# Kernel tuning notes

Measured on AMD Instinct MI355X. Metric: run time of the kernel, lower is better.

## Reference

```python
import jax, jax.numpy as jnp
import numpy as np

IN_CH, OUT_CH, HEADS, DIM = 256, 256, 8, 64

def _xavier(key, shape, fan_in, fan_out):
    upper = np.sqrt(6.0) / np.sqrt(float(fan_in + fan_out))
    return jax.random.uniform(key, shape, jnp.float32) * (2.0 * upper) - upper

def setup_inputs() -> dict:
    key = jax.random.key(0)
    kf, kq, kk, kv, ko = jax.random.split(key, 5)
    features = jax.random.normal(kf, (8, 1024, IN_CH), jnp.float32)
    weight_q = _xavier(kq, (IN_CH, HEADS, DIM), IN_CH, HEADS * DIM)
    weight_k = _xavier(kk, (IN_CH, HEADS, DIM), IN_CH, HEADS * DIM)
    weight_v = _xavier(kv, (IN_CH, HEADS, DIM), IN_CH, HEADS * DIM)
    weight_out = _xavier(ko, (OUT_CH, HEADS, DIM), HEADS * DIM, OUT_CH)
    return {"features": features, "weight_q": weight_q, "weight_k": weight_k,
            "weight_v": weight_v, "weight_out": weight_out}

def reference(features, weight_q, weight_k, weight_v, weight_out):
    # QKV projections: (b,n,c) x (c,h,d) -> (b,n,h,d)
    q = jnp.einsum('bnc,chd->bnhd', features, weight_q)
    k = jnp.einsum('bnc,chd->bnhd', features, weight_k)
    v = jnp.einsum('bnc,chd->bnhd', features, weight_v)
    # Scores: (b, i=query, j=key, h)
    qk = jnp.einsum('bihd,bjhd->bijh', q, k) / jnp.sqrt(jnp.asarray(DIM, q.dtype))
    # NOTE: original softmaxes over dim=1, i.e. the QUERY axis (faithful quirk)
    qk_softmax = jax.nn.softmax(qk, axis=1)
    # Original broadcasts v over j, so combination = v[b,i,h,d] * sum_j softmax[b,i,j,h]
    attn_weight = jnp.sum(qk_softmax, axis=2)  # (b, i, h)
    applied = v * attn_weight[:, :, :, None]   # (b, i, h, d)
    out = jnp.einsum('bihd,ohd->bio', applied, weight_out)
    return out
```

## Files before the change

### kernel.cpp

```cpp
#include <hip/hip_runtime.h>
#include <hip/hip_bf16.h>
#include <cstdint>


typedef __attribute__((ext_vector_type(8))) short bf16x8;
typedef __attribute__((ext_vector_type(4))) float f32x4;

#define EXP2(x) __builtin_amdgcn_exp2f(x)
#define MFMA(a, b, c) __builtin_amdgcn_mfma_f32_16x16x32_bf16((a), (b), (c), 0, 0, 0)
#define QSCALE 0.18033688011112042f

static __device__ __forceinline__ uint32_t pk2(float x, float y) {
  union { __hip_bfloat162 h; uint32_t u; } c;
  c.h = __float22bfloat162_rn(float2{x, y});
  return c.u;
}
static __device__ __forceinline__ short cvt1(float f) {
  union { __hip_bfloat16 h; short s; } c;
  c.h = __float2bfloat16(f);
  return c.s;
}

__global__ __launch_bounds__(256) void k_prep(
    const float* __restrict__ F,  const float* __restrict__ Wq,
    const float* __restrict__ Wk, const float* __restrict__ Wv,
    const float* __restrict__ Wo,
    short* __restrict__ Fb, short* __restrict__ Wtf, short* __restrict__ Wobf)
{
  const int gt = blockIdx.x * 256 + threadIdx.x;
  if (gt < 262144) {
    const int b  = gt >> 15;
    const int r  = gt & 32767;
    const int c8 = r & 31;
    const int i  = r >> 5;
    const float* src = F + ((size_t)(b * 1024 + i)) * 256 + c8 * 8;
    const float4 v0 = *(const float4*)src;
    const float4 v1 = *(const float4*)(src + 4);
    uint32_t u[4] = {pk2(v0.x, v0.y), pk2(v0.z, v0.w),
                     pk2(v1.x, v1.y), pk2(v1.z, v1.w)};
    const int strip = i >> 4, lo = i & 15;
    const int s = c8 >> 3, kk = (c8 >> 2) & 1, hi = c8 & 3;
    *(uint4*)&Fb[(size_t)b * 262144 + (size_t)strip * 4096 + s * 1024 +
                 kk * 512 + (hi * 16 + lo) * 8] = *(uint4*)u;
  } else if (gt < 311296) {
    const int wt = gt - 262144;
    const int m  = wt >> 14;
    const int r  = wt & 16383;
    const int n  = r & 511;
    const int c8 = r >> 9;
    const float* W = (m == 0) ? Wq : (m == 1) ? Wk : Wv;
    const float scale = (m == 0) ? QSCALE : 1.0f;
    short tmp[8];
#pragma unroll
    for (int j = 0; j < 8; ++j)
      tmp[j] = cvt1(W[(size_t)(c8 * 8 + j) * 512 + n] * scale);
    const int h = n >> 6, fm = (n >> 4) & 3, lo = n & 15;
    const int s = c8 >> 3, kk = (c8 >> 2) & 1, hi = c8 & 3;
    *(int4*)&Wtf[(size_t)(((m * 8 + h) * 4 + fm) * 4 + s) * 1024 +
                 kk * 512 + (hi * 16 + lo) * 8] = *(int4*)tmp;
  } else if (gt < 327680) {
    const int wo = gt - 311296;
    const int o  = wo >> 6;
    const int k8 = wo & 63;
    const float* src = Wo + (size_t)o * 512 + k8 * 8;
    const float4 v0 = *(const float4*)src;
    const float4 v1 = *(const float4*)(src + 4);
    uint32_t u[4] = {pk2(v0.x, v0.y), pk2(v0.z, v0.w),
                     pk2(v1.x, v1.y), pk2(v1.z, v1.w)};
    const int nt = o >> 6, fc = (o >> 4) & 3, lo = o & 15;
    const int s = k8 >> 3, kk = (k8 >> 2) & 1, hi = k8 & 3;
    *(uint4*)&Wobf[(size_t)((nt * 4 + fc) * 8 + s) * 1024 +
                   kk * 512 + (hi * 16 + lo) * 8] = *(uint4*)u;
  }
}

__global__ __launch_bounds__(256, 4) void k_qkv(
    const short* __restrict__ Fb, const short* __restrict__ Wtf,
    short* __restrict__ Qf, short* __restrict__ Kf, short* __restrict__ Vf)
{
  const int hw = blockIdx.x, t = threadIdx.x;
  const int xcd  = hw & 7;
  const int slot = hw >> 3;
  const int mh   = slot >> 3;
  const int g    = xcd * 8 + (slot & 7);
  const int m    = mh >> 3;
  const int h    = mh & 7;
  const int b    = g >> 3;
  const int mt   = g & 7;
  const int wv = t >> 6, l = t & 63, lo = l & 15, hi = l >> 4;

  f32x4 acc[4][2];
#pragma unroll
  for (int i = 0; i < 4; ++i)
#pragma unroll
    for (int j = 0; j < 2; ++j) acc[i][j] = (f32x4){0.f, 0.f, 0.f, 0.f};

  const short* fbase = Fb + (size_t)b * 262144;
  const short* wbase = Wtf + (size_t)(m * 8 + h) * 16384;
  const int strip0 = mt * 8 + wv * 2;

#pragma unroll
  for (int s = 0; s < 4; ++s) {
    bf16x8 bb[2][2];
#pragma unroll
    for (int fn = 0; fn < 2; ++fn)
#pragma unroll
      for (int kk = 0; kk < 2; ++kk)
        bb[fn][kk] = *(const bf16x8*)(fbase + (size_t)(strip0 + fn) * 4096 +
                                      s * 1024 + kk * 512 + l * 8);
#pragma unroll
    for (int fm = 0; fm < 4; ++fm) {
      const short* wr = wbase + (size_t)(fm * 4 + s) * 1024 + l * 8;
      bf16x8 a0 = *(const bf16x8*)(wr);
      bf16x8 a1 = *(const bf16x8*)(wr + 512);
      acc[fm][0] = MFMA(a0, bb[0][0], acc[fm][0]);
      acc[fm][1] = MFMA(a0, bb[1][0], acc[fm][1]);
      acc[fm][0] = MFMA(a1, bb[0][1], acc[fm][0]);
      acc[fm][1] = MFMA(a1, bb[1][1], acc[fm][1]);
    }
  }

  short* O = (m == 0) ? Qf : (m == 1) ? Kf : Vf;
  const size_t obase = (size_t)(b * 8 + h) * 65536;
#pragma unroll
  for (int fm = 0; fm < 4; ++fm)
#pragma unroll
    for (int fn = 0; fn < 2; ++fn) {
      uint32_t u[2] = {pk2(acc[fm][fn][0], acc[fm][fn][1]),
                       pk2(acc[fm][fn][2], acc[fm][fn][3])};
      const int strip = strip0 + fn;
      const int kk = fm >> 1;
      const int hip = (fm & 1) * 2 + (hi >> 1);
      const int e0 = (hi & 1) * 4;
      *(uint2*)&O[obase + (size_t)strip * 1024 + kk * 512 +
                  (hip * 16 + lo) * 8 + e0] = *(uint2*)u;
    }
}

template <int NSLICE>
__global__ __launch_bounds__(256, 4) void k_attw(
    const short* __restrict__ Qf, const short* __restrict__ Kf,
    float* __restrict__ Wgp)
{
  constexpr int JW = 1024 / NSLICE;
  constexpr int NS = JW / 16;
  __shared__ float Red[4 * JW];
  const int hw = blockIdx.x, t = threadIdx.x;
  const int xcd  = hw & 7;
  const int slot = hw >> 3;
  const int bh   = xcd * 8 + slot / NSLICE;
  const int jb   = slot % NSLICE;
  const size_t base = (size_t)bh * 65536;
  const int wv = t >> 6, l = t & 63, lo = l & 15, hi = l >> 4;
  const short* qb = Qf + base;
  const short* kb = Kf + base;

  bf16x8 bk[NS][2];
#pragma unroll
  for (int js = 0; js < NS; ++js) {
    const short* kr = kb + (size_t)(jb * NS + js) * 1024 + l * 8;
    bk[js][0] = *(const bf16x8*)(kr);
    bk[js][1] = *(const bf16x8*)(kr + 512);
  }

  float cs[NS];
#pragma unroll
  for (int js = 0; js < NS; ++js) cs[js] = 0.f;

  {
    bf16x8 a0[2], a1[2];
#pragma unroll
    for (int p = 0; p < 2; ++p) {
      const short* q = qb + (size_t)(wv + 4 * p) * 1024 + l * 8;
      a0[p] = *(const bf16x8*)(q);
      a1[p] = *(const bf16x8*)(q + 512);
    }
#pragma unroll 1
    for (int k = 0; k < 8; ++k) {
      bf16x8 n0[2], n1[2];
      if (k < 7) {
#pragma unroll
        for (int p = 0; p < 2; ++p) {
          const short* q = qb + (size_t)(wv + 8 * (k + 1) + 4 * p) * 1024 + l * 8;
          n0[p] = *(const bf16x8*)(q);
          n1[p] = *(const bf16x8*)(q + 512);
        }
      }
#pragma unroll
      for (int js = 0; js < NS; ++js) {
#pragma unroll
        for (int p = 0; p < 2; ++p) {
          f32x4 acc = (f32x4){0.f, 0.f, 0.f, 0.f};
          acc = MFMA(a0[p], bk[js][0], acc);
          acc = MFMA(a1[p], bk[js][1], acc);
#pragma unroll
          for (int r = 0; r < 4; ++r) cs[js] += EXP2(acc[r]);
        }
      }
      if (k < 7) {
#pragma unroll
        for (int p = 0; p < 2; ++p) { a0[p] = n0[p]; a1[p] = n1[p]; }
      }
    }
  }

#pragma unroll
  for (int js = 0; js < NS; ++js) {
    cs[js] += __shfl_xor(cs[js], 16, 64);
    cs[js] += __shfl_xor(cs[js], 32, 64);
  }
  if (hi == 0) {
#pragma unroll
    for (int js = 0; js < NS; ++js) Red[wv * JW + js * 16 + lo] = cs[js];
  }
  __syncthreads();
  if (t < JW) {
    float d = Red[t] + Red[JW + t] + Red[2 * JW + t] + Red[3 * JW + t];
    Red[t] = __builtin_amdgcn_rcpf(d);
  }
  __syncthreads();
  float rjv[NS][4];
#pragma unroll
  for (int js = 0; js < NS; ++js)
#pragma unroll
    for (int r = 0; r < 4; ++r)
      rjv[js][r] = Red[js * 16 + hi * 4 + r];

  {
    bf16x8 a0[2], a1[2];
#pragma unroll
    for (int p = 0; p < 2; ++p) {
      const short* q = qb + (size_t)(wv + 4 * p) * 1024 + l * 8;
      a0[p] = *(const bf16x8*)(q);
      a1[p] = *(const bf16x8*)(q + 512);
    }
#pragma unroll 1
    for (int k = 0; k < 8; ++k) {
      bf16x8 n0[2], n1[2];
      if (k < 7) {
#pragma unroll
        for (int p = 0; p < 2; ++p) {
          const short* q = qb + (size_t)(wv + 8 * (k + 1) + 4 * p) * 1024 + l * 8;
          n0[p] = *(const bf16x8*)(q);
          n1[p] = *(const bf16x8*)(q + 512);
        }
      }
      float w2[2] = {0.f, 0.f};
#pragma unroll
      for (int js = 0; js < NS; ++js) {
#pragma unroll
        for (int p = 0; p < 2; ++p) {
          f32x4 acc = (f32x4){0.f, 0.f, 0.f, 0.f};
          acc = MFMA(bk[js][0], a0[p], acc);
          acc = MFMA(bk[js][1], a1[p], acc);
#pragma unroll
          for (int r = 0; r < 4; ++r)
            w2[p] = fmaf(EXP2(acc[r]), rjv[js][r], w2[p]);
        }
      }
#pragma unroll
      for (int p = 0; p < 2; ++p) {
        w2[p] += __shfl_xor(w2[p], 16, 64);
        w2[p] += __shfl_xor(w2[p], 32, 64);
      }
      if (l < 16) {
#pragma unroll
        for (int p = 0; p < 2; ++p)
          Wgp[(size_t)jb * 65536 + (size_t)bh * 1024 +
              (wv + 8 * k + 4 * p) * 16 + l] = w2[p];
      }
      if (k < 7) {
#pragma unroll
        for (int p = 0; p < 2; ++p) { a0[p] = n0[p]; a1[p] = n1[p]; }
      }
    }
  }
}

template <int NSLICE>
__global__ __launch_bounds__(256, 2) void k_out(
    const short* __restrict__ Vf, const float* __restrict__ Wgp,
    const short* __restrict__ Wobf, float* __restrict__ Out)
{
  __shared__ float Wl[8][64];
  const int hw = blockIdx.x, t = threadIdx.x;
  const int slot = hw >> 3;
  const int g    = (hw & 7) * 16 + (slot >> 2);
  const int nt   = slot & 3;
  const int b    = g >> 4;
  const int mt   = g & 15;
  const int n0   = nt * 64;
  const int m0   = mt * 64;
  const int wv = t >> 6, l = t & 63, lo = l & 15, hi = l >> 4;

#pragma unroll
  for (int e = t; e < 512; e += 256) {
    int s = e >> 6, i2 = e & 63;
    float sum = 0.f;
#pragma unroll
    for (int p = 0; p < NSLICE; ++p)
      sum += Wgp[(size_t)p * 65536 + (size_t)(b * 8 + s) * 1024 + m0 + i2];
    Wl[s][i2] = sum;
  }
  __syncthreads();

  f32x4 acc[4];
#pragma unroll
  for (int j = 0; j < 4; ++j) acc[j] = (f32x4){0.f, 0.f, 0.f, 0.f};

  const int strip = mt * 4 + wv;

#pragma unroll 1
  for (int s = 0; s < 8; ++s) {
    const float w = Wl[s][wv * 16 + lo];
    const short* vt = Vf + (size_t)(b * 8 + s) * 65536 + (size_t)strip * 1024;
#pragma unroll
    for (int kk = 0; kk < 2; ++kk) {
      int4 raw = *(const int4*)(vt + kk * 512 + l * 8);
      uint32_t* u = (uint32_t*)&raw;
      uint32_t o[4];
#pragma unroll
      for (int j = 0; j < 4; ++j) {
        float f0 = __uint_as_float(u[j] << 16) * w;
        float f1 = __uint_as_float(u[j] & 0xffff0000u) * w;
        o[j] = pk2(f0, f1);
      }
      bf16x8 a = *(bf16x8*)o;
#pragma unroll
      for (int fc = 0; fc < 4; ++fc) {
        bf16x8 bfr = *(const bf16x8*)(Wobf + (size_t)((nt * 4 + fc) * 8 + s) * 1024 +
                                      kk * 512 + l * 8);
        acc[fc] = MFMA(a, bfr, acc[fc]);
      }
    }
  }

#pragma unroll
  for (int fc = 0; fc < 4; ++fc)
#pragma unroll
    for (int r = 0; r < 4; ++r) {
      int i = m0 + wv * 16 + hi * 4 + r;
      int o = n0 + fc * 16 + lo;
      Out[(size_t)(b * 1024 + i) * 256 + o] = acc[fc][r];
    }
}

extern "C" void kernel_launch(void* const* d_in, const int* in_sizes, int n_in,
                              void* d_out, int out_size, void* d_ws, size_t ws_size,
                              hipStream_t stream) {
  const float* F  = (const float*)d_in[0];
  const float* Wq = (const float*)d_in[1];
  const float* Wk = (const float*)d_in[2];
  const float* Wv = (const float*)d_in[3];
  const float* Wo = (const float*)d_in[4];
  float* out = (float*)d_out;

  char* ws = (char*)d_ws;
  short* Qf   = (short*)(ws);
  short* Kf   = (short*)(ws + (size_t)(8  << 20));
  short* Vf   = (short*)(ws + (size_t)(16 << 20));
  short* Fb   = (short*)(ws + (size_t)(24 << 20));
  float* Wgp  = (float*)(ws + (size_t)(28 << 20));
  short* Wtf  = (short*)(ws + (size_t)(32 << 20));
  short* Wobf = (short*)(ws + (size_t)(32 << 20) + (768 << 10));

  k_prep<<<dim3(1280), 256, 0, stream>>>(F, Wq, Wk, Wv, Wo, Fb, Wtf, Wobf);
  k_qkv <<<dim3(1536), 256, 0, stream>>>(Fb, Wtf, Qf, Kf, Vf);
  k_attw<16><<<dim3(1024), 256, 0, stream>>>(Qf, Kf, Wgp);
  k_out<16> <<<dim3(512),  256, 0, stream>>>(Vf, Wgp, Wobf, out);
}
```

Baseline: 58.07 us.

## Cache exp scores in LDS instead of recomputing QK in second pass

Result: no change. 57.22 us (median of 3 runs) (-1.5%).

```diff
diff --git a/kernel.cpp b/kernel.cpp
--- a/kernel.cpp
+++ b/kernel.cpp
@@ -138,12 +138,13 @@
 }
 
 template <int NSLICE>
-__global__ __launch_bounds__(256, 4) void k_attw(
+__global__ __launch_bounds__(256, 2) void k_attw(
     const short* __restrict__ Qf, const short* __restrict__ Kf,
     float* __restrict__ Wgp)
 {
   constexpr int JW = 1024 / NSLICE;
   constexpr int NS = JW / 16;
+  __shared__ short E[JW][1032];
   __shared__ float Red[4 * JW];
   const int hw = blockIdx.x, t = threadIdx.x;
   const int xcd  = hw & 7;
@@ -193,8 +194,12 @@
           f32x4 acc = (f32x4){0.f, 0.f, 0.f, 0.f};
           acc = MFMA(a0[p], bk[js][0], acc);
           acc = MFMA(a1[p], bk[js][1], acc);
-#pragma unroll
-          for (int r = 0; r < 4; ++r) cs[js] += EXP2(acc[r]);
+          float e0 = EXP2(acc[0]), e1 = EXP2(acc[1]);
+          float e2 = EXP2(acc[2]), e3 = EXP2(acc[3]);
+          cs[js] += (e0 + e1) + (e2 + e3);
+          uint32_t u[2] = {pk2(e0, e1), pk2(e2, e3)};
+          const int strip = wv + 8 * k + 4 * p;
+          *(uint2*)&E[js * 16 + lo][strip * 16 + hi * 4] = *(uint2*)u;
         }
       }
       if (k < 7) {
@@ -219,61 +224,21 @@
     Red[t] = __builtin_amdgcn_rcpf(d);
   }
   __syncthreads();
-  float rjv[NS][4];
-#pragma unroll
-  for (int js = 0; js < NS; ++js)
-#pragma unroll
-    for (int r = 0; r < 4; ++r)
-      rjv[js][r] = Red[js * 16 + hi * 4 + r];
 
   {
-    bf16x8 a0[2], a1[2];
-#pragma unroll
-    for (int p = 0; p < 2; ++p) {
-      const short* q = qb + (size_t)(wv + 4 * p) * 1024 + l * 8;
-      a0[p] = *(const bf16x8*)(q);
-      a1[p] = *(const bf16x8*)(q + 512);
-    }
-#pragma unroll 1
-    for (int k = 0; k < 8; ++k) {
-      bf16x8 n0[2], n1[2];
-      if (k < 7) {
-#pragma unroll
-        for (int p = 0; p < 2; ++p) {
-          const short* q = qb + (size_t)(wv + 8 * (k + 1) + 4 * p) * 1024 + l * 8;
-          n0[p] = *(const bf16x8*)(q);
-          n1[p] = *(const bf16x8*)(q + 512);
-        }
-      }
-      float w2[2] = {0.f, 0.f};
-#pragma unroll
-      for (int js = 0; js < NS; ++js) {
-#pragma unroll
-        for (int p = 0; p < 2; ++p) {
-          f32x4 acc = (f32x4){0.f, 0.f, 0.f, 0.f};
-          acc = MFMA(bk[js][0], a0[p], acc);
-          acc = MFMA(bk[js][1], a1[p], acc);
-#pragma unroll
-          for (int r = 0; r < 4; ++r)
-            w2[p] = fmaf(EXP2(acc[r]), rjv[js][r], w2[p]);
-        }
-      }
-#pragma unroll
-      for (int p = 0; p < 2; ++p) {
-        w2[p] += __shfl_xor(w2[p], 16, 64);
-        w2[p] += __shfl_xor(w2[p], 32, 64);
-      }
-      if (l < 16) {
-#pragma unroll
-        for (int p = 0; p < 2; ++p)
-          Wgp[(size_t)jb * 65536 + (size_t)bh * 1024 +
-              (wv + 8 * k + 4 * p) * 16 + l] = w2[p];
-      }
-      if (k < 7) {
-#pragma unroll
-        for (int p = 0; p < 2; ++p) { a0[p] = n0[p]; a1[p] = n1[p]; }
-      }
-    }
+    const int i0 = t * 4;
+    float w4[4] = {0.f, 0.f, 0.f, 0.f};
+#pragma unroll
+    for (int j = 0; j < JW; ++j) {
+      const float rjj = Red[j];
+      uint2 u = *(const uint2*)&E[j][i0];
+      w4[0] = fmaf(__uint_as_float(u.x << 16),          rjj, w4[0]);
+      w4[1] = fmaf(__uint_as_float(u.x & 0xffff0000u),  rjj, w4[1]);
+      w4[2] = fmaf(__uint_as_float(u.y << 16),          rjj, w4[2]);
+      w4[3] = fmaf(__uint_as_float(u.y & 0xffff0000u),  rjj, w4[3]);
+    }
+    float4 o = {w4[0], w4[1], w4[2], w4[3]};
+    *(float4*)&Wgp[(size_t)jb * 65536 + (size_t)bh * 1024 + i0] = o;
   }
 }
 
@@ -361,11 +326,11 @@
   short* Vf   = (short*)(ws + (size_t)(16 << 20));
   short* Fb   = (short*)(ws + (size_t)(24 << 20));
   float* Wgp  = (float*)(ws + (size_t)(28 << 20));
-  short* Wtf  = (short*)(ws + (size_t)(32 << 20));
-  short* Wobf = (short*)(ws + (size_t)(32 << 20) + (768 << 10));
+  short* Wtf  = (short*)(ws + (size_t)(36 << 20));
+  short* Wobf = (short*)(ws + (size_t)(36 << 20) + (768 << 10));
 
   k_prep<<<dim3(1280), 256, 0, stream>>>(F, Wq, Wk, Wv, Wo, Fb, Wtf, Wobf);
   k_qkv <<<dim3(1536), 256, 0, stream>>>(Fb, Wtf, Qf, Kf, Vf);
-  k_attw<16><<<dim3(1024), 256, 0, stream>>>(Qf, Kf, Wgp);
-  k_out<16> <<<dim3(512),  256, 0, stream>>>(Vf, Wgp, Wobf, out);
-}
+  k_attw<32><<<dim3(2048), 256, 0, stream>>>(Qf, Kf, Wgp);
+  k_out<32> <<<dim3(512),  256, 0, stream>>>(Vf, Wgp, Wobf, out);
+}
```
